# Kernel optimization log

Hardware: AMD Instinct MI355X
Metric: run time of the kernel (lower is better)

## Reference

```python
import jax, jax.numpy as jnp
import numpy as np

N = 100000   # nodes
E = 1600000  # edges (before self-loops)
H = 128      # in_channels == hidden_channels
G = 64       # graphs in batch


def setup_inputs() -> dict:
    key = jax.random.key(0)
    ks = jax.random.split(key, 12)
    s = 1.0 / np.sqrt(H)
    inp = {
        "x": jax.random.normal(ks[0], (N, H), jnp.float32),
        "edge_weight": jax.random.uniform(ks[1], (E,), jnp.float32),
        "edge_index": jax.random.randint(ks[2], (2, E), 0, N, dtype=jnp.int64),
        "batch": jnp.sort(jax.random.randint(ks[3], (N,), 0, G, dtype=jnp.int64)),
        "W1": jax.random.uniform(ks[4], (H, H), jnp.float32, -s, s),
        "b1": jnp.zeros((H,), jnp.float32),
        "W2": jax.random.uniform(ks[5], (H, H), jnp.float32, -s, s),
        "b2": jnp.zeros((H,), jnp.float32),
        "W3": jax.random.uniform(ks[6], (H, H), jnp.float32, -s, s),
        "b3": jnp.zeros((H,), jnp.float32),
        "lin_w": jax.random.uniform(ks[7], (H, 1), jnp.float32, -s, s),
        "lin_b": jax.random.uniform(ks[8], (1,), jnp.float32, -s, s),
    }
    return inp


def reference(x, edge_weight, W1, b1, W2, b2, W3, b3, lin_w, lin_b, edge_index, batch):
    # PyG GCNConv with add_self_loops=True, symmetric normalization.
    loops = jnp.arange(N, dtype=edge_index.dtype)
    row = jnp.concatenate([edge_index[0], loops])  # source
    col = jnp.concatenate([edge_index[1], loops])  # target
    ew = jnp.concatenate([edge_weight, jnp.ones((N,), edge_weight.dtype)])

    deg = jax.ops.segment_sum(ew, col, num_segments=N)          # in-degree (weighted)
    safe = jnp.where(deg > 0, deg, 1.0)
    dinv = jnp.where(deg > 0, jax.lax.rsqrt(safe), 0.0)
    norm = dinv[row] * ew * dinv[col]                            # [E+N]

    def conv(h, W, b):
        h = h @ W                                                # [N,H] dense transform
        msg = h[row] * norm[:, None]                             # gather + scale
        return jax.ops.segment_sum(msg, col, num_segments=N) + b # scatter-add

    h = jax.nn.relu(conv(x, W1, b1))
    h = jax.nn.relu(conv(h, W2, b2))
    h = jax.nn.relu(conv(h, W3, b3))

    # global_mean_pool over graph ids
    sums = jax.ops.segment_sum(h, batch, num_segments=G)         # [G,H]
    cnts = jax.ops.segment_sum(jnp.ones((N,), h.dtype), batch, num_segments=G)
    pooled = sums / jnp.maximum(cnts, 1.0)[:, None]
    # dropout is identity at inference
    return pooled @ lin_w + lin_b                                # [G,1]
```

## Files before the change

### kernel.cpp

```cpp
#include <hip/hip_runtime.h>
#include <stdint.h>

#define N_NODES 100000
#define N_EDGES 1600000
#define HDIM    128
#define G_GRAPHS 64
#define NTOT (N_EDGES + N_NODES)
#define PSLOTS 64
#define NSTRIPS (N_NODES / 16)
#define NTB 1024
#define NDB ((N_EDGES + 2047) / 2048)
#define BSH 9
#define NBK ((N_NODES + 511) / 512)
#define MAXBKT 10240

static_assert(N_NODES % 16 == 0, "tile/agg");
static_assert(N_NODES < (1 << 17), "src fits 17 bits");

typedef __attribute__((ext_vector_type(8))) short bf16x8;
typedef __attribute__((ext_vector_type(4))) float f32x4;
typedef __attribute__((ext_vector_type(2))) float f32x2;

__device__ __forceinline__ uint32_t f2bf(float x) {
    uint32_t b = __float_as_uint(x);
    return (b + 0x7FFFu + ((b >> 16) & 1u)) >> 16;
}
__device__ __forceinline__ uint32_t pack2(float lo, float hi) {
    return f2bf(lo) | (f2bf(hi) << 16);
}

#define FXSCALE 1099511627776.0f

__global__ void k_wswz(const float* __restrict__ Wa, const float* __restrict__ Wb,
                       const float* __restrict__ Wc, uint16_t* __restrict__ dst) {
    int gi = blockIdx.x * 256 + threadIdx.x;
    int w = gi >> 14, idx = gi & 16383;
    const float* src = (w == 0) ? Wa : (w == 1) ? Wb : Wc;
    int k = idx >> 7, n = idx & 127;
    int kc = k >> 5, kq = (k >> 3) & 3, j = k & 7;
    int nt = n >> 4, nl = n & 15;
    dst[w * 16384 + (((kc * 8 + nt) * 64) + kq * 16 + nl) * 8 + j] = (uint16_t)f2bf(src[idx]);
}

__device__ __forceinline__ bf16x8 load_row_f32(const float* p) {
    float4 a = ((const float4*)p)[0];
    float4 b = ((const float4*)p)[1];
    union { uint32_t u[4]; bf16x8 v; } c;
    c.u[0] = pack2(a.x, a.y); c.u[1] = pack2(a.z, a.w);
    c.u[2] = pack2(b.x, b.y); c.u[3] = pack2(b.z, b.w);
    return c.v;
}

__device__ __forceinline__ void transform_body_l1(int tb, int nTB, int tid,
                                                  const float* __restrict__ hin,
                                                  const bf16x8* __restrict__ Wfrag,
                                                  uint32_t* __restrict__ t) {
    int lane = tid & 63;
    int quad = lane >> 4;
    int mrow = lane & 15;
    int gwave = tb * 4 + (tid >> 6);
    int nwaves = nTB * 4;
    for (int strip = gwave; strip < NSTRIPS; strip += nwaves) {
        const float* hrow = hin + ((size_t)(strip * 16 + mrow)) * 128 + quad * 8;
        bf16x8 A0 = load_row_f32(hrow);
        bf16x8 A1 = load_row_f32(hrow + 32);
        bf16x8 A2 = load_row_f32(hrow + 64);
        bf16x8 A3 = load_row_f32(hrow + 96);
        f32x4 acc[8];
#pragma unroll
        for (int nt = 0; nt < 8; nt++) {
            f32x4 a = {0.f, 0.f, 0.f, 0.f};
            a = __builtin_amdgcn_mfma_f32_16x16x32_bf16(A0, Wfrag[(0 * 8 + nt) * 64 + lane], a, 0, 0, 0);
            a = __builtin_amdgcn_mfma_f32_16x16x32_bf16(A1, Wfrag[(1 * 8 + nt) * 64 + lane], a, 0, 0, 0);
            a = __builtin_amdgcn_mfma_f32_16x16x32_bf16(A2, Wfrag[(2 * 8 + nt) * 64 + lane], a, 0, 0, 0);
            a = __builtin_amdgcn_mfma_f32_16x16x32_bf16(A3, Wfrag[(3 * 8 + nt) * 64 + lane], a, 0, 0, 0);
            acc[nt] = a;
        }
#pragma unroll
        for (int nt = 0; nt < 8; nt++) {
#pragma unroll
            for (int r = 0; r < 4; r++) {
                float v = acc[nt][r];
                float nb = __shfl_xor(v, 1);
                int s16 = __builtin_amdgcn_cvt_pk_fp8_f32(v, nb, 0, false);
                int hi  = __shfl_xor(s16, 2);
                if (!(lane & 3)) {
                    int orow = strip * 16 + quad * 4 + r;
                    int oc = (nt * 16 + mrow) >> 2;
                    t[(size_t)orow * 32 + oc] = (uint32_t)(s16 & 0xffff) | ((uint32_t)hi << 16);
                }
            }
        }
    }
}

__global__ __launch_bounds__(256) void k_tr_count(
        const int* __restrict__ ei, const float* __restrict__ x,
        const bf16x8* __restrict__ Wfrag, uint32_t* __restrict__ t,
        int* __restrict__ partials) {
    __shared__ int hist[NBK];
    int bi = blockIdx.x;
    int q7 = bi / 7, r7 = bi % 7;
    int tq = q7 * 4 + r7;
    bool isT = (r7 < 4) && (tq < NTB);
    int tid = threadIdx.x;
    if (isT) {
        transform_body_l1(tq, NTB, tid, x, Wfrag, t);
    } else {
        int nTbef = q7 * 4 + (r7 < 4 ? r7 : 4);
        if (nTbef > NTB) nTbef = NTB;
        int db = bi - nTbef;
        for (int i = tid; i < NBK; i += 256) hist[i] = 0;
        __syncthreads();
        int e0 = db * 2048 + tid;
#pragma unroll
        for (int k = 0; k < 8; k++) {
            int e = e0 + k * 256;
            if (e < N_EDGES) atomicAdd(&hist[ei[N_EDGES + e] >> BSH], 1);
        }
        __syncthreads();
        for (int i = tid; i < NBK; i += 256) partials[i * NDB + db] = hist[i];
    }
}

__global__ void k_bscan(const int* __restrict__ partials, int* __restrict__ blockBase,
                        int* __restrict__ totals) {
    int b = blockIdx.x, tid = threadIdx.x;
    int v[4]; int s = 0;
#pragma unroll
    for (int j = 0; j < 4; j++) {
        int i = tid * 4 + j;
        v[j] = (i < NDB) ? partials[b * NDB + i] : 0;
        s += v[j];
    }
    __shared__ int sm[256];
    sm[tid] = s; __syncthreads();
    for (int off = 1; off < 256; off <<= 1) {
        int u = 0; if (tid >= off) u = sm[tid - off];
        __syncthreads(); sm[tid] += u; __syncthreads();
    }
    int run = sm[tid] - s;
#pragma unroll
    for (int j = 0; j < 4; j++) {
        int i = tid * 4 + j;
        if (i < NDB) blockBase[b * NDB + i] = run;
        run += v[j];
    }
    if (tid == 255) totals[b] = sm[255];
}

__global__ void k_starts(const int* __restrict__ totals, int* __restrict__ bstart) {
    int tid = threadIdx.x;
    int v = (tid < NBK) ? totals[tid] : 0;
    __shared__ int sm[256];
    sm[tid] = v; __syncthreads();
    for (int off = 1; off < 256; off <<= 1) {
        int u = 0; if (tid >= off) u = sm[tid - off];
        __syncthreads(); sm[tid] += u; __syncthreads();
    }
    if (tid < NBK) bstart[tid] = sm[tid] - v;
    if (tid == 255) bstart[NBK] = sm[255];
}

__global__ __launch_bounds__(256) void k_scatter(
        const int* __restrict__ ei, const float* __restrict__ ew,
        const int* __restrict__ blockBase, const int* __restrict__ bstart,
        uint2* __restrict__ recs) {
    __shared__ int hist[NBK];
    __shared__ int basesh[NBK];
    int tid = threadIdx.x, db = blockIdx.x;
    for (int i = tid; i < NBK; i += 256) {
        hist[i] = 0;
        basesh[i] = bstart[i] + blockBase[i * NDB + db];
    }
    __syncthreads();
    int e0 = db * 2048 + tid;
#pragma unroll
    for (int k = 0; k < 8; k++) {
        int e = e0 + k * 256;
        if (e < N_EDGES) {
            int src = ei[e];
            int dst = ei[N_EDGES + e];
            float w = ew[e];
            int bkt = dst >> BSH;
            int r = atomicAdd(&hist[bkt], 1);
            recs[basesh[bkt] + r] =
                make_uint2((uint32_t)src | ((uint32_t)(dst & 511) << 17),
                           __float_as_uint(w));
        }
    }
}

__global__ __launch_bounds__(256) void k_build(
        const uint2* __restrict__ recs, const int* __restrict__ bstart,
        int* __restrict__ cnt, float* __restrict__ dinv, int* __restrict__ offs,
        int2* __restrict__ csr) {
    __shared__ unsigned long long acc[512];
    __shared__ uint16_t rk[MAXBKT];
    __shared__ int loff[512];
    __shared__ int sm[256];
    int b = blockIdx.x, tid = threadIdx.x;
    int e0 = bstart[b], ne = bstart[b + 1] - e0;
    for (int i = tid; i < 512; i += 256) acc[i] = 0ULL;
    __syncthreads();
    for (int j = tid; j < ne; j += 256) {
        uint2 rc = recs[e0 + j];
        int dl = (rc.x >> 17) & 511;
        float w = __uint_as_float(rc.y);
        unsigned long long pk = (1ULL << 48) | (unsigned long long)(w * FXSCALE);
        unsigned long long old = atomicAdd(&acc[dl], pk);
        rk[j] = (uint16_t)(old >> 48);
    }
    __syncthreads();
    int nb0 = b << BSH;
    int nreal = N_NODES - nb0; if (nreal > 512) nreal = 512;
    int i0 = tid * 2, i1 = tid * 2 + 1;
    int c0 = (i0 < nreal) ? (int)(acc[i0] >> 48) + 1 : 0;
    int c1 = (i1 < nreal) ? (int)(acc[i1] >> 48) + 1 : 0;
    sm[tid] = c0 + c1;
    __syncthreads();
    for (int off = 1; off < 256; off <<= 1) {
        int u = 0; if (tid >= off) u = sm[tid - off];
        __syncthreads(); sm[tid] += u; __syncthreads();
    }
    int run = e0 + nb0 + (sm[tid] - (c0 + c1));
    loff[i0] = run;
    loff[i1] = run + c0;
    if (i0 < nreal) {
        unsigned long long pk = acc[i0];
        int c = (int)(pk >> 48);
        float deg = (float)(pk & ((1ULL << 48) - 1)) * (1.0f / FXSCALE);
        cnt[nb0 + i0] = c;
        offs[nb0 + i0] = run;
        dinv[nb0 + i0] = 1.0f / sqrtf(deg + 1.0f);
        csr[run + c] = make_int2(nb0 + i0, __float_as_int(1.0f));
    }
    if (i1 < nreal) {
        unsigned long long pk = acc[i1];
        int c = (int)(pk >> 48);
        float deg = (float)(pk & ((1ULL << 48) - 1)) * (1.0f / FXSCALE);
        cnt[nb0 + i1] = c;
        offs[nb0 + i1] = run + c0;
        dinv[nb0 + i1] = 1.0f / sqrtf(deg + 1.0f);
        csr[run + c0 + c] = make_int2(nb0 + i1, __float_as_int(1.0f));
    }
    __syncthreads();
    for (int j = tid; j < ne; j += 256) {
        uint2 rc = recs[e0 + j];
        int dl = (rc.x >> 17) & 511;
        int src = rc.x & 0x1ffff;
        csr[loff[dl] + rk[j]] = make_int2(src, (int)rc.y);
    }
}

__global__ void k_norm(int2* __restrict__ csr, const float* __restrict__ dinv) {
    int p = blockIdx.x * 256 + threadIdx.x;
    if (p < NTOT) {
        int2 c = csr[p];
        csr[p].y = __float_as_int(__int_as_float(c.y) * dinv[c.x]);
    }
}

__device__ __forceinline__ void fetch8(const char* __restrict__ tb, int g4, int lq8,
                                       int base, uint32_t osrc, float wsrc,
                                       uint2 (&va)[8], float (&wf)[8]) {
#pragma unroll
    for (int k = 0; k < 8; k++) {
        int o  = __builtin_amdgcn_ds_bpermute(g4 + base + 4 * k, (int)osrc);
        int wb = __builtin_amdgcn_ds_bpermute(g4 + base + 4 * k, __float_as_int(wsrc));
        wf[k] = __uint_as_float((uint32_t)wb);
        va[k] = *(const uint2*)(tb + (uint32_t)(o + lq8));
    }
}

__device__ __forceinline__ void acc8(const uint2 (&va)[8], const float (&wf)[8],
                                     f32x2& p0, f32x2& p1, f32x2& p2, f32x2& p3) {
#pragma unroll
    for (int k = 0; k < 8; k++) {
        f32x2 lo0 = __builtin_amdgcn_cvt_pk_f32_fp8((int)va[k].x, false);
        f32x2 hi0 = __builtin_amdgcn_cvt_pk_f32_fp8((int)va[k].x, true);
        f32x2 lo1 = __builtin_amdgcn_cvt_pk_f32_fp8((int)va[k].y, false);
        f32x2 hi1 = __builtin_amdgcn_cvt_pk_f32_fp8((int)va[k].y, true);
        f32x2 wp = { wf[k], wf[k] };
        p0 += wp * lo0; p1 += wp * hi0; p2 += wp * lo1; p3 += wp * hi1;
    }
}

__device__ __forceinline__ void aggregate_node(const char* __restrict__ tb,
        const int2* __restrict__ csr, int beg, int num, int ql, int g4, int lq8,
        f32x2& p0, f32x2& p1, f32x2& p2, f32x2& p3) {
    int2 m0 = make_int2(0, 0), m1 = make_int2(0, 0);
    if (ql < num) m0 = csr[beg + ql];
    if (ql + 16 < num) m1 = csr[beg + 16 + ql];
    uint32_t o0 = (uint32_t)m0.x << 7;
    uint32_t o1 = (uint32_t)m1.x << 7;
    float w0 = __int_as_float(m0.y), w1 = __int_as_float(m1.y);
    bool c1 = num > 8, c2 = num > 16, c3 = num > 24;
    uint2 va[8], vb[8], vc[8], vd[8];
    float wa[8], wb[8], wc[8], wd[8];
    fetch8(tb, g4, lq8, 0, o0, w0, va, wa);
    if (c1) fetch8(tb, g4, lq8, 32, o0, w0, vb, wb);
    acc8(va, wa, p0, p1, p2, p3);
    if (c2) fetch8(tb, g4, lq8, 0, o1, w1, vc, wc);
    if (c1) acc8(vb, wb, p0, p1, p2, p3);
    if (c3) fetch8(tb, g4, lq8, 32, o1, w1, vd, wd);
    if (c2) acc8(vc, wc, p0, p1, p2, p3);
    if (c3) acc8(vd, wd, p0, p1, p2, p3);
    for (int base = 32; base < num; base += 16) {
        int2 mm = make_int2(0, 0);
        if (base + ql < num) mm = csr[beg + base + ql];
        uint32_t oo = (uint32_t)mm.x << 7;
        float mws = __int_as_float(mm.y);
        bool h = base + 8 < num;
        fetch8(tb, g4, lq8, 0, oo, mws, va, wa);
        if (h) fetch8(tb, g4, lq8, 32, oo, mws, vb, wb);
        acc8(va, wa, p0, p1, p2, p3);
        if (h) acc8(vb, wb, p0, p1, p2, p3);
    }
}

__device__ __forceinline__ f32x2 relu2(f32x2 p, float dn, f32x2 b) {
    f32x2 r;
    r.x = fmaxf(p.x * dn + b.x, 0.f);
    r.y = fmaxf(p.y * dn + b.y, 0.f);
    return r;
}

__global__ __launch_bounds__(256) void k_agg_tr(
        const uint32_t* __restrict__ tin, const int* __restrict__ offs,
        const int* __restrict__ cnt, const int2* __restrict__ csr,
        const float* __restrict__ dinv, const float* __restrict__ bias,
        const bf16x8* __restrict__ Wfrag, uint32_t* __restrict__ tout) {
    __shared__ uint32_t ht[16 * 16 * 4];
    int tid = threadIdx.x;
    int lane = tid & 63;
    int ql = lane & 15;
    int grp = lane & 48;
    int g4 = grp << 2, lq8 = ql << 3;
    int row = (tid >> 6) * 4 + (lane >> 4);
    int node = blockIdx.x * 16 + row;
    int beg = offs[node];
    int num = cnt[node] + 1;
    float dn = dinv[node];
    f32x2 p0 = {0.f, 0.f}, p1 = {0.f, 0.f}, p2 = {0.f, 0.f}, p3 = {0.f, 0.f};
    aggregate_node((const char*)tin, csr, beg, num, ql, g4, lq8, p0, p1, p2, p3);
    const f32x2* bp = (const f32x2*)bias;
    p0 = relu2(p0, dn, bp[ql * 4 + 0]);
    p1 = relu2(p1, dn, bp[ql * 4 + 1]);
    p2 = relu2(p2, dn, bp[ql * 4 + 2]);
    p3 = relu2(p3, dn, bp[ql * 4 + 3]);
    {
        int slot = (ql + row) & 15;
        uint32_t* dst = &ht[(row * 16 + slot) * 4];
        dst[0] = pack2(p0.x, p0.y);
        dst[1] = pack2(p1.x, p1.y);
        dst[2] = pack2(p2.x, p2.y);
        dst[3] = pack2(p3.x, p3.y);
    }
    __syncthreads();
    int quad = lane >> 4;
    int m = lane & 15;
    int wid = tid >> 6;
    bf16x8 A[4];
#pragma unroll
    for (int c = 0; c < 4; c++) {
        int sl = (c * 4 + quad + m) & 15;
        A[c] = *(const bf16x8*)&ht[(m * 16 + sl) * 4];
    }
    int strip = blockIdx.x;
#pragma unroll
    for (int u = 0; u < 2; u++) {
        int nt = wid * 2 + u;
        f32x4 a = {0.f, 0.f, 0.f, 0.f};
        a = __builtin_amdgcn_mfma_f32_16x16x32_bf16(A[0], Wfrag[(0 * 8 + nt) * 64 + lane], a, 0, 0, 0);
        a = __builtin_amdgcn_mfma_f32_16x16x32_bf16(A[1], Wfrag[(1 * 8 + nt) * 64 + lane], a, 0, 0, 0);
        a = __builtin_amdgcn_mfma_f32_16x16x32_bf16(A[2], Wfrag[(2 * 8 + nt) * 64 + lane], a, 0, 0, 0);
        a = __builtin_amdgcn_mfma_f32_16x16x32_bf16(A[3], Wfrag[(3 * 8 + nt) * 64 + lane], a, 0, 0, 0);
#pragma unroll
        for (int r = 0; r < 4; r++) {
            float v = a[r];
            float nb = __shfl_xor(v, 1);
            int s16 = __builtin_amdgcn_cvt_pk_fp8_f32(v, nb, 0, false);
            int hi  = __shfl_xor(s16, 2);
            if (!(lane & 3)) {
                int orow = strip * 16 + quad * 4 + r;
                int oc = (nt * 16 + m) >> 2;
                tout[(size_t)orow * 32 + oc] = (uint32_t)(s16 & 0xffff) | ((uint32_t)hi << 16);
            }
        }
    }
}

__global__ __launch_bounds__(256) void k_agg_pool(
        const uint32_t* __restrict__ t, const int* __restrict__ offs,
        const int* __restrict__ cnt, const int2* __restrict__ csr,
        const float* __restrict__ dinv, const float* __restrict__ bias,
        const float* __restrict__ lw, const int* __restrict__ batch,
        float* __restrict__ pp) {
    int tid = threadIdx.x;
    int lane = tid & 63;
    int ql = lane & 15;
    int grp = lane & 48;
    int g4 = grp << 2, lq8 = ql << 3;
    int node = blockIdx.x * 16 + (tid >> 6) * 4 + (lane >> 4);
    int beg = offs[node];
    int num = cnt[node] + 1;
    float dn = dinv[node];
    f32x2 p0 = {0.f, 0.f}, p1 = {0.f, 0.f}, p2 = {0.f, 0.f}, p3 = {0.f, 0.f};
    aggregate_node((const char*)t, csr, beg, num, ql, g4, lq8, p0, p1, p2, p3);
    const f32x2* bp = (const f32x2*)bias;
    p0 = relu2(p0, dn, bp[ql * 4 + 0]);
    p1 = relu2(p1, dn, bp[ql * 4 + 1]);
    p2 = relu2(p2, dn, bp[ql * 4 + 2]);
    p3 = relu2(p3, dn, bp[ql * 4 + 3]);
    const f32x2* wp2 = (const f32x2*)lw;
    f32x2 q0 = wp2[ql * 4 + 0], q1 = wp2[ql * 4 + 1];
    f32x2 q2 = wp2[ql * 4 + 2], q3 = wp2[ql * 4 + 3];
    float d = p0.x * q0.x + p0.y * q0.y + p1.x * q1.x + p1.y * q1.y
            + p2.x * q2.x + p2.y * q2.y + p3.x * q3.x + p3.y * q3.y;
    for (int off = 8; off; off >>= 1) d += __shfl_down(d, off);
    if (ql == 0)
        atomicAdd(&pp[(blockIdx.x & (PSLOTS - 1)) * G_GRAPHS + batch[node]], d);
}

__global__ void k_final(const float* __restrict__ pp, const int* __restrict__ batch,
                        const float* __restrict__ lb, float* __restrict__ out) {
    int g = threadIdx.x;
    float s = 0.f;
#pragma unroll
    for (int k = 0; k < PSLOTS; k++) s += pp[k * G_GRAPHS + g];
    int lo = 0, hi = N_NODES;
    while (lo < hi) { int m = (lo + hi) >> 1; if (batch[m] < g) lo = m + 1; else hi = m; }
    int beg = lo;
    hi = N_NODES;
    while (lo < hi) { int m = (lo + hi) >> 1; if (batch[m] < g + 1) lo = m + 1; else hi = m; }
    float c = fmaxf((float)(lo - beg), 1.0f);
    out[g] = s / c + lb[0];
}

extern "C" void kernel_launch(void* const* d_in, const int* in_sizes, int n_in,
                              void* d_out, int out_size, void* d_ws, size_t ws_size,
                              hipStream_t stream) {
    const float* x   = (const float*)d_in[0];
    const float* ew  = (const float*)d_in[1];
    const int*   ei  = (const int*)d_in[2];
    const int*   bat = (const int*)d_in[3];
    const float* W1  = (const float*)d_in[4];
    const float* b1  = (const float*)d_in[5];
    const float* W2  = (const float*)d_in[6];
    const float* b2  = (const float*)d_in[7];
    const float* W3  = (const float*)d_in[8];
    const float* b3  = (const float*)d_in[9];
    const float* lw  = (const float*)d_in[10];
    const float* lb  = (const float*)d_in[11];
    float* out = (float*)d_out;

    char* w = (char*)d_ws;
    size_t o = 0;
    auto carve = [&](size_t bytes) -> void* {
        void* p = w + o;
        o = (o + bytes + 255) & ~(size_t)255;
        return p;
    };
    float*    pp     = (float*)carve((size_t)PSLOTS * G_GRAPHS * 4);
    int*      parts  = (int*)  carve((size_t)NBK * NDB * 4);
    int*      bbase  = (int*)  carve((size_t)NBK * NDB * 4);
    int*      totals = (int*)  carve((size_t)NBK * 4);
    int*      bstart = (int*)  carve((size_t)(NBK + 1) * 4);
    uint2*    recs   = (uint2*)carve((size_t)N_EDGES * 8);
    int*      cnt    = (int*)  carve((size_t)N_NODES * 4);
    float*    dinv   = (float*)carve((size_t)N_NODES * 4);
    int*      offs   = (int*)  carve((size_t)N_NODES * 4);
    int2*     csr    = (int2*) carve((size_t)NTOT * 8);
    uint32_t* tA     = (uint32_t*)carve((size_t)N_NODES * 128);
    uint32_t* tB     = (uint32_t*)carve((size_t)N_NODES * 128);
    uint16_t* wsz    = (uint16_t*)carve((size_t)3 * 16384 * 2);
    (void)ws_size; (void)in_sizes; (void)n_in; (void)out_size;

    hipMemsetAsync(pp, 0, (size_t)PSLOTS * G_GRAPHS * 4, stream);

    k_wswz<<<192, 256, 0, stream>>>(W1, W2, W3, wsz);
    k_tr_count<<<NTB + NDB, 256, 0, stream>>>(ei, x, (const bf16x8*)wsz, tA, parts);
    k_bscan<<<NBK, 256, 0, stream>>>(parts, bbase, totals);
    k_starts<<<1, 256, 0, stream>>>(totals, bstart);
    k_scatter<<<NDB, 256, 0, stream>>>(ei, ew, bbase, bstart, recs);
    k_build<<<NBK, 256, 0, stream>>>(recs, bstart, cnt, dinv, offs, csr);
    k_norm<<<(NTOT + 255) / 256, 256, 0, stream>>>(csr, dinv);

    k_agg_tr<<<NSTRIPS, 256, 0, stream>>>(tA, offs, cnt, csr, dinv, b1,
                                          (const bf16x8*)(wsz + 16384), tB);
    k_agg_tr<<<NSTRIPS, 256, 0, stream>>>(tB, offs, cnt, csr, dinv, b2,
                                          (const bf16x8*)(wsz + 2 * 16384), tA);
    k_agg_pool<<<NSTRIPS, 256, 0, stream>>>(tA, offs, cnt, csr, dinv, b3, lw, bat, pp);

    k_final<<<1, G_GRAPHS, 0, stream>>>(pp, bat, lb, out);
}
```

Baseline: 334.2 us.

## Make aggregation kernels persistent with software-prefetch of next strip's CSR metadata

The three aggregation kernels now launch a fixed grid of persistent blocks that loop over 16-node strips with a grid stride. Each iteration prefetches the next strip's offsets, counts, dinv and first CSR entries while the current strip's gathers are in flight, and bias and linear weights are loaded once per block. The aim is to hide the dependent-load latency at the start of each strip and cut block launch overhead. In exchange it adds a second __syncthreads per iteration, more registers, and static work assignment that may balance poorly across CUs when node degrees vary.

```diff
diff --git a/kernel.cpp b/kernel.cpp
--- a/kernel.cpp
+++ b/kernel.cpp
@@ -13,6 +13,7 @@
 #define BSH 9
 #define NBK ((N_NODES + 511) / 512)
 #define MAXBKT 10240
+#define AGRID 1568
 
 static_assert(N_NODES % 16 == 0, "tile/agg");
 static_assert(N_NODES < (1 << 17), "src fits 17 bits");
@@ -286,12 +287,13 @@
     }
 }
 
-__device__ __forceinline__ void aggregate_node(const char* __restrict__ tb,
-        const int2* __restrict__ csr, int beg, int num, int ql, int g4, int lq8,
+__device__ __forceinline__ void agg_pipe(const char* __restrict__ tb,
+        const int2* __restrict__ csr, int beg, int num, int2 m0, int2 m1,
+        int ql, int g4, int lq8,
+        const int* __restrict__ offs, const int* __restrict__ cnt,
+        const float* __restrict__ dinv, int nnode,
+        int& nbeg, int& nnum, float& ndn, int2& n0, int2& n1,
         f32x2& p0, f32x2& p1, f32x2& p2, f32x2& p3) {
-    int2 m0 = make_int2(0, 0), m1 = make_int2(0, 0);
-    if (ql < num) m0 = csr[beg + ql];
-    if (ql + 16 < num) m1 = csr[beg + 16 + ql];
     uint32_t o0 = (uint32_t)m0.x << 7;
     uint32_t o1 = (uint32_t)m1.x << 7;
     float w0 = __int_as_float(m0.y), w1 = __int_as_float(m1.y);
@@ -300,6 +302,9 @@
     float wa[8], wb[8], wc[8], wd[8];
     fetch8(tb, g4, lq8, 0, o0, w0, va, wa);
     if (c1) fetch8(tb, g4, lq8, 32, o0, w0, vb, wb);
+    nbeg = offs[nnode];
+    nnum = cnt[nnode] + 1;
+    ndn  = dinv[nnode];
     acc8(va, wa, p0, p1, p2, p3);
     if (c2) fetch8(tb, g4, lq8, 0, o1, w1, vc, wc);
     if (c1) acc8(vb, wb, p0, p1, p2, p3);
@@ -317,6 +322,9 @@
         acc8(va, wa, p0, p1, p2, p3);
         if (h) acc8(vb, wb, p0, p1, p2, p3);
     }
+    n0 = make_int2(0, 0); n1 = make_int2(0, 0);
+    if (ql < nnum) n0 = csr[nbeg + ql];
+    if (ql + 16 < nnum) n1 = csr[nbeg + 16 + ql];
 }
 
 __device__ __forceinline__ f32x2 relu2(f32x2 p, float dn, f32x2 b) {
@@ -338,56 +346,74 @@
     int grp = lane & 48;
     int g4 = grp << 2, lq8 = ql << 3;
     int row = (tid >> 6) * 4 + (lane >> 4);
-    int node = blockIdx.x * 16 + row;
+    int quad = lane >> 4;
+    int m = lane & 15;
+    int wid = tid >> 6;
+    const f32x2* bp = (const f32x2*)bias;
+    f32x2 b0 = bp[ql * 4 + 0], b1 = bp[ql * 4 + 1];
+    f32x2 b2 = bp[ql * 4 + 2], b3 = bp[ql * 4 + 3];
+    int strip = blockIdx.x;
+    if (strip >= NSTRIPS) return;
+    int node = strip * 16 + row;
     int beg = offs[node];
     int num = cnt[node] + 1;
     float dn = dinv[node];
-    f32x2 p0 = {0.f, 0.f}, p1 = {0.f, 0.f}, p2 = {0.f, 0.f}, p3 = {0.f, 0.f};
-    aggregate_node((const char*)tin, csr, beg, num, ql, g4, lq8, p0, p1, p2, p3);
-    const f32x2* bp = (const f32x2*)bias;
-    p0 = relu2(p0, dn, bp[ql * 4 + 0]);
-    p1 = relu2(p1, dn, bp[ql * 4 + 1]);
-    p2 = relu2(p2, dn, bp[ql * 4 + 2]);
-    p3 = relu2(p3, dn, bp[ql * 4 + 3]);
-    {
-        int slot = (ql + row) & 15;
-        uint32_t* dst = &ht[(row * 16 + slot) * 4];
-        dst[0] = pack2(p0.x, p0.y);
-        dst[1] = pack2(p1.x, p1.y);
-        dst[2] = pack2(p2.x, p2.y);
-        dst[3] = pack2(p3.x, p3.y);
-    }
-    __syncthreads();
-    int quad = lane >> 4;
-    int m = lane & 15;
-    int wid = tid >> 6;
-    bf16x8 A[4];
-#pragma unroll
-    for (int c = 0; c < 4; c++) {
-        int sl = (c * 4 + quad + m) & 15;
-        A[c] = *(const bf16x8*)&ht[(m * 16 + sl) * 4];
-    }
-    int strip = blockIdx.x;
-#pragma unroll
-    for (int u = 0; u < 2; u++) {
-        int nt = wid * 2 + u;
-        f32x4 a = {0.f, 0.f, 0.f, 0.f};
-        a = __builtin_amdgcn_mfma_f32_16x16x32_bf16(A[0], Wfrag[(0 * 8 + nt) * 64 + lane], a, 0, 0, 0);
-        a = __builtin_amdgcn_mfma_f32_16x16x32_bf16(A[1], Wfrag[(1 * 8 + nt) * 64 + lane], a, 0, 0, 0);
-        a = __builtin_amdgcn_mfma_f32_16x16x32_bf16(A[2], Wfrag[(2 * 8 + nt) * 64 + lane], a, 0, 0, 0);
-        a = __builtin_amdgcn_mfma_f32_16x16x32_bf16(A[3], Wfrag[(3 * 8 + nt) * 64 + lane], a, 0, 0, 0);
-#pragma unroll
-        for (int r = 0; r < 4; r++) {
-            float v = a[r];
-            float nb = __shfl_xor(v, 1);
-            int s16 = __builtin_amdgcn_cvt_pk_fp8_f32(v, nb, 0, false);
-            int hi  = __shfl_xor(s16, 2);
-            if (!(lane & 3)) {
-                int orow = strip * 16 + quad * 4 + r;
-                int oc = (nt * 16 + m) >> 2;
-                tout[(size_t)orow * 32 + oc] = (uint32_t)(s16 & 0xffff) | ((uint32_t)hi << 16);
+    int2 m0 = make_int2(0, 0), m1 = make_int2(0, 0);
+    if (ql < num) m0 = csr[beg + ql];
+    if (ql + 16 < num) m1 = csr[beg + 16 + ql];
+    while (true) {
+        int nstrip = strip + AGRID;
+        bool hasnext = nstrip < NSTRIPS;
+        int nnode = hasnext ? nstrip * 16 + row : node;
+        int nbeg, nnum; float ndn; int2 n0, n1;
+        f32x2 p0 = {0.f, 0.f}, p1 = {0.f, 0.f}, p2 = {0.f, 0.f}, p3 = {0.f, 0.f};
+        agg_pipe((const char*)tin, csr, beg, num, m0, m1, ql, g4, lq8,
+                 offs, cnt, dinv, nnode, nbeg, nnum, ndn, n0, n1,
+                 p0, p1, p2, p3);
+        p0 = relu2(p0, dn, b0);
+        p1 = relu2(p1, dn, b1);
+        p2 = relu2(p2, dn, b2);
+        p3 = relu2(p3, dn, b3);
+        {
+            int slot = (ql + row) & 15;
+            uint32_t* dst = &ht[(row * 16 + slot) * 4];
+            dst[0] = pack2(p0.x, p0.y);
+            dst[1] = pack2(p1.x, p1.y);
+            dst[2] = pack2(p2.x, p2.y);
+            dst[3] = pack2(p3.x, p3.y);
+        }
+        __syncthreads();
+        bf16x8 A[4];
+#pragma unroll
+        for (int c = 0; c < 4; c++) {
+            int sl = (c * 4 + quad + m) & 15;
+            A[c] = *(const bf16x8*)&ht[(m * 16 + sl) * 4];
+        }
+        __syncthreads();
+#pragma unroll
+        for (int u = 0; u < 2; u++) {
+            int nt = wid * 2 + u;
+            f32x4 a = {0.f, 0.f, 0.f, 0.f};
+            a = __builtin_amdgcn_mfma_f32_16x16x32_bf16(A[0], Wfrag[(0 * 8 + nt) * 64 + lane], a, 0, 0, 0);
+            a = __builtin_amdgcn_mfma_f32_16x16x32_bf16(A[1], Wfrag[(1 * 8 + nt) * 64 + lane], a, 0, 0, 0);
+            a = __builtin_amdgcn_mfma_f32_16x16x32_bf16(A[2], Wfrag[(2 * 8 + nt) * 64 + lane], a, 0, 0, 0);
+            a = __builtin_amdgcn_mfma_f32_16x16x32_bf16(A[3], Wfrag[(3 * 8 + nt) * 64 + lane], a, 0, 0, 0);
+#pragma unroll
+            for (int r = 0; r < 4; r++) {
+                float v = a[r];
+                float nb = __shfl_xor(v, 1);
+                int s16 = __builtin_amdgcn_cvt_pk_fp8_f32(v, nb, 0, false);
+                int hi  = __shfl_xor(s16, 2);
+                if (!(lane & 3)) {
+                    int orow = strip * 16 + quad * 4 + r;
+                    int oc = (nt * 16 + m) >> 2;
+                    tout[(size_t)orow * 32 + oc] = (uint32_t)(s16 & 0xffff) | ((uint32_t)hi << 16);
+                }
             }
         }
+        if (!hasnext) break;
+        strip = nstrip; node = nnode;
+        beg = nbeg; num = nnum; dn = ndn; m0 = n0; m1 = n1;
     }
 }
 
@@ -402,25 +428,44 @@
     int ql = lane & 15;
     int grp = lane & 48;
     int g4 = grp << 2, lq8 = ql << 3;
-    int node = blockIdx.x * 16 + (tid >> 6) * 4 + (lane >> 4);
+    int row = (tid >> 6) * 4 + (lane >> 4);
+    const f32x2* bp = (const f32x2*)bias;
+    f32x2 b0 = bp[ql * 4 + 0], b1 = bp[ql * 4 + 1];
+    f32x2 b2 = bp[ql * 4 + 2], b3 = bp[ql * 4 + 3];
+    const f32x2* wp2 = (const f32x2*)lw;
+    f32x2 q0 = wp2[ql * 4 + 0], q1 = wp2[ql * 4 + 1];
+    f32x2 q2 = wp2[ql * 4 + 2], q3 = wp2[ql * 4 + 3];
+    int strip = blockIdx.x;
+    if (strip >= NSTRIPS) return;
+    int node = strip * 16 + row;
     int beg = offs[node];
     int num = cnt[node] + 1;
     float dn = dinv[node];
-    f32x2 p0 = {0.f, 0.f}, p1 = {0.f, 0.f}, p2 = {0.f, 0.f}, p3 = {0.f, 0.f};
-    aggregate_node((const char*)t, csr, beg, num, ql, g4, lq8, p0, p1, p2, p3);
-    const f32x2* bp = (const f32x2*)bias;
-    p0 = relu2(p0, dn, bp[ql * 4 + 0]);
-    p1 = relu2(p1, dn, bp[ql * 4 + 1]);
-    p2 = relu2(p2, dn, bp[ql * 4 + 2]);
-    p3 = relu2(p3, dn, bp[ql * 4 + 3]);
-    const f32x2* wp2 = (const f32x2*)lw;
-    f32x2 q0 = wp2[ql * 4 + 0], q1 = wp2[ql * 4 + 1];
-    f32x2 q2 = wp2[ql * 4 + 2], q3 = wp2[ql * 4 + 3];
-    float d = p0.x * q0.x + p0.y * q0.y + p1.x * q1.x + p1.y * q1.y
-            + p2.x * q2.x + p2.y * q2.y + p3.x * q3.x + p3.y * q3.y;
-    for (int off = 8; off; off >>= 1) d += __shfl_down(d, off);
-    if (ql == 0)
-        atomicAdd(&pp[(blockIdx.x & (PSLOTS - 1)) * G_GRAPHS + batch[node]], d);
+    int2 m0 = make_int2(0, 0), m1 = make_int2(0, 0);
+    if (ql < num) m0 = csr[beg + ql];
+    if (ql + 16 < num) m1 = csr[beg + 16 + ql];
+    while (true) {
+        int nstrip = strip + AGRID;
+        bool hasnext = nstrip < NSTRIPS;
+        int nnode = hasnext ? nstrip * 16 + row : node;
+        int nbeg, nnum; float ndn; int2 n0, n1;
+        f32x2 p0 = {0.f, 0.f}, p1 = {0.f, 0.f}, p2 = {0.f, 0.f}, p3 = {0.f, 0.f};
+        agg_pipe((const char*)t, csr, beg, num, m0, m1, ql, g4, lq8,
+                 offs, cnt, dinv, nnode, nbeg, nnum, ndn, n0, n1,
+                 p0, p1, p2, p3);
+        p0 = relu2(p0, dn, b0);
+        p1 = relu2(p1, dn, b1);
+        p2 = relu2(p2, dn, b2);
+        p3 = relu2(p3, dn, b3);
+        float d = p0.x * q0.x + p0.y * q0.y + p1.x * q1.x + p1.y * q1.y
+                + p2.x * q2.x + p2.y * q2.y + p3.x * q3.x + p3.y * q3.y;
+        for (int off = 8; off; off >>= 1) d += __shfl_down(d, off);
+        if (ql == 0)
+            atomicAdd(&pp[(strip & (PSLOTS - 1)) * G_GRAPHS + batch[node]], d);
+        if (!hasnext) break;
+        strip = nstrip; node = nnode;
+        beg = nbeg; num = nnum; dn = ndn; m0 = n0; m1 = n1;
+    }
 }
 
 __global__ void k_final(const float* __restrict__ pp, const int* __restrict__ batch,
@@ -487,11 +532,11 @@
     k_build<<<NBK, 256, 0, stream>>>(recs, bstart, cnt, dinv, offs, csr);
     k_norm<<<(NTOT + 255) / 256, 256, 0, stream>>>(csr, dinv);
 
-    k_agg_tr<<<NSTRIPS, 256, 0, stream>>>(tA, offs, cnt, csr, dinv, b1,
-                                          (const bf16x8*)(wsz + 16384), tB);
-    k_agg_tr<<<NSTRIPS, 256, 0, stream>>>(tB, offs, cnt, csr, dinv, b2,
-                                          (const bf16x8*)(wsz + 2 * 16384), tA);
-    k_agg_pool<<<NSTRIPS, 256, 0, stream>>>(tA, offs, cnt, csr, dinv, b3, lw, bat, pp);
+    k_agg_tr<<<AGRID, 256, 0, stream>>>(tA, offs, cnt, csr, dinv, b1,
+                                        (const bf16x8*)(wsz + 16384), tB);
+    k_agg_tr<<<AGRID, 256, 0, stream>>>(tB, offs, cnt, csr, dinv, b2,
+                                        (const bf16x8*)(wsz + 2 * 16384), tA);
+    k_agg_pool<<<AGRID, 256, 0, stream>>>(tA, offs, cnt, csr, dinv, b3, lw, bat, pp);
 
     k_final<<<1, G_GRAPHS, 0, stream>>>(pp, bat, lb, out);
 }
```

After: 348.5 us. +4.3%, slower.
